# Kernel optimization log

Hardware: AMD Instinct MI355X
Metric: run time of the kernel (lower is better)

The kernel has to match this reference:

```python
import jax, jax.numpy as jnp
import numpy as np

MAX_SEQ_LEN = 128
H = 512
B = 256
S = 128
VOCAB = MAX_SEQ_LEN + 2
SOS = MAX_SEQ_LEN  # start token index in embedding table


def _lstm_cell(x, h, c, w_ih, w_hh, b):
    # PyTorch gate order: i, f, g, o
    z = x @ w_ih.T + h @ w_hh.T + b
    i, f, g, o = jnp.split(z, 4, axis=-1)
    c = jax.nn.sigmoid(f) * c + jax.nn.sigmoid(i) * jnp.tanh(g)
    h = jax.nn.sigmoid(o) * jnp.tanh(c)
    return h, c


def _run_layer(xs, w_ih, w_hh, b):
    nb = xs.shape[1]
    h0 = jnp.zeros((nb, H), xs.dtype)

    def step(carry, x):
        h, c = carry
        h, c = _lstm_cell(x, h, c, w_ih, w_hh, b)
        return (h, c), h

    (hT, cT), ys = jax.lax.scan(step, (h0, h0), xs)
    return ys, hT, cT


def _forward(l2_features, enc, dec, emb, fc1_w, fc1_b, fc2_w, fc2_b, fc3_w, mlp):
    xs = jnp.transpose(l2_features, (1, 0, 2))  # [S,B,F]
    hs, cs = [], []
    for (w_ih, w_hh, b) in enc:  # 3-layer encoder LSTM
        xs, hT, cT = _run_layer(xs, w_ih, w_hh, b)
        hs.append(hT)
        cs.append(cT)
    enc_outs = xs  # [S,B,H]
    h_stack = jnp.stack(hs)  # [3,B,H]
    c_stack = jnp.stack(cs)
    ot = enc_outs @ fc2_w.T + fc2_b  # [S,B,256], loop-invariant
    w1, b1, w2, b2, w3, b3 = mlp
    (dw_ih0, dw_hh0, db0), (dw_ih1, dw_hh1, db1), (dw_ih2, dw_hh2, db2) = dec
    nb = l2_features.shape[0]
    tok0 = jnp.full((nb,), SOS, dtype=jnp.int32)
    ctx0 = jnp.zeros((nb, H), l2_features.dtype)

    def dec_step(carry, _):
        h, c, ctx, tok = carry
        # dropout is identity in eval mode
        x = jnp.concatenate([emb[tok], ctx], axis=1)  # [B, 2H]
        h0, c0 = _lstm_cell(x, h[0], c[0], dw_ih0, dw_hh0, db0)
        h1, c1 = _lstm_cell(h0, h[1], c[1], dw_ih1, dw_hh1, db1)
        h2, c2 = _lstm_cell(h1, h[2], c[2], dw_ih2, dw_hh2, db2)
        ht = h2 @ fc1_w.T + fc1_b  # [B,256]
        scores = jnp.tanh(ot + ht[None]) @ fc3_w[0]  # [S,B]
        w = jax.nn.softmax(scores, axis=0)  # softmax over encoder time (dim 0)
        new_ctx = jnp.einsum('sb,sbd->bd', w, enc_outs)  # [B,H]
        hdd = jax.nn.relu(jnp.concatenate([h2, new_ctx], axis=1) @ w1.T + b1)
        hdd = jax.nn.relu(hdd @ w2.T + b2)
        out = hdd @ w3.T + b3  # [B, MAX_SEQ_LEN]
        new_tok = jnp.argmax(out, axis=-1).astype(jnp.int32)
        new_carry = (jnp.stack([h0, h1, h2]), jnp.stack([c0, c1, c2]), new_ctx, new_tok)
        return new_carry, out

    _, outs = jax.lax.scan(dec_step, (h_stack, c_stack, ctx0, tok0), None, length=MAX_SEQ_LEN)
    return outs  # [MAX_SEQ_LEN, B, MAX_SEQ_LEN]


def setup_inputs() -> dict:
    key = jax.random.key(0)
    ks = iter(jax.random.split(key, 40))

    def p(shape):
        return jax.random.normal(next(ks), shape, dtype=jnp.float32) * 0.05

    d = {"l2_features": jax.random.normal(next(ks), (B, S, MAX_SEQ_LEN), dtype=jnp.float32)}
    d["enc_w_ih0"] = p((4 * H, MAX_SEQ_LEN)); d["enc_w_hh0"] = p((4 * H, H)); d["enc_b0"] = p((4 * H,))
    d["enc_w_ih1"] = p((4 * H, H)); d["enc_w_hh1"] = p((4 * H, H)); d["enc_b1"] = p((4 * H,))
    d["enc_w_ih2"] = p((4 * H, H)); d["enc_w_hh2"] = p((4 * H, H)); d["enc_b2"] = p((4 * H,))
    d["dec_w_ih0"] = p((4 * H, 2 * H)); d["dec_w_hh0"] = p((4 * H, H)); d["dec_b0"] = p((4 * H,))
    d["dec_w_ih1"] = p((4 * H, H)); d["dec_w_hh1"] = p((4 * H, H)); d["dec_b1"] = p((4 * H,))
    d["dec_w_ih2"] = p((4 * H, H)); d["dec_w_hh2"] = p((4 * H, H)); d["dec_b2"] = p((4 * H,))
    d["emb"] = p((VOCAB, H))
    d["fc1_w"] = p((256, H)); d["fc1_b"] = p((256,))
    d["fc2_w"] = p((256, H)); d["fc2_b"] = p((256,))
    d["fc3_w"] = p((1, 256))
    d["mlp_w1"] = p((512, 1024)); d["mlp_b1"] = p((512,))
    d["mlp_w2"] = p((256, 512)); d["mlp_b2"] = p((256,))
    d["mlp_w3"] = p((MAX_SEQ_LEN, 256)); d["mlp_b3"] = p((MAX_SEQ_LEN,))
    return d


def reference(l2_features, enc_w_ih0, enc_w_hh0, enc_b0, enc_w_ih1, enc_w_hh1, enc_b1,
              enc_w_ih2, enc_w_hh2, enc_b2, dec_w_ih0, dec_w_hh0, dec_b0,
              dec_w_ih1, dec_w_hh1, dec_b1, dec_w_ih2, dec_w_hh2, dec_b2,
              emb, fc1_w, fc1_b, fc2_w, fc2_b, fc3_w,
              mlp_w1, mlp_b1, mlp_w2, mlp_b2, mlp_w3, mlp_b3):
    enc = ((enc_w_ih0, enc_w_hh0, enc_b0), (enc_w_ih1, enc_w_hh1, enc_b1), (enc_w_ih2, enc_w_hh2, enc_b2))
    dec = ((dec_w_ih0, dec_w_hh0, dec_b0), (dec_w_ih1, dec_w_hh1, dec_b1), (dec_w_ih2, dec_w_hh2, dec_b2))
    mlp = (mlp_w1, mlp_b1, mlp_w2, mlp_b2, mlp_w3, mlp_b3)
    return _forward(l2_features, enc, dec, emb, fc1_w, fc1_b, fc2_w, fc2_b, fc3_w, mlp)
```

## Files before the change

### kernel.cpp

```cpp
#include <hip/hip_runtime.h>

#define BB 256
#define SS 128
#define FDIM 128
#define HH 512
#define H4 2048
#define TDEC 128
#define SOS_TOK 128

typedef short short8 __attribute__((ext_vector_type(8)));
typedef float f32x4 __attribute__((ext_vector_type(4)));

__device__ __forceinline__ float sigf(float x){ return 1.0f/(1.0f+__expf(-x)); }
__device__ __forceinline__ float tanh_f(float x){ return 1.0f - 2.0f/(__expf(2.0f*x)+1.0f); }

__device__ __forceinline__ void split3(float x, unsigned& h, unsigned& m, unsigned& l){
    union { float f; unsigned u; } a; a.f = x;
    h = (a.u + 0x7fffu + ((a.u>>16)&1u)) >> 16;
    union { unsigned u; float f; } hf; hf.u = h << 16;
    float r1 = x - hf.f;
    union { float f; unsigned u; } b; b.f = r1;
    m = (b.u + 0x7fffu + ((b.u>>16)&1u)) >> 16;
    union { unsigned u; float f; } mf; mf.u = m << 16;
    float r2 = r1 - mf.f;
    union { float f; unsigned u; } c; c.f = r2;
    l = (c.u + 0x7fffu + ((c.u>>16)&1u)) >> 16;
}

__device__ __forceinline__ void splitw8(float4 v, uint2& H, uint2& M, uint2& L){
    unsigned h0,m0,l0,h1,m1,l1,h2,m2,l2,h3,m3,l3;
    split3(v.x,h0,m0,l0); split3(v.y,h1,m1,l1); split3(v.z,h2,m2,l2); split3(v.w,h3,m3,l3);
    H.x = h0 | (h1<<16); H.y = h2 | (h3<<16);
    M.x = m0 | (m1<<16); M.y = m2 | (m3<<16);
    L.x = l0 | (l1<<16); L.y = l2 | (l3<<16);
}

__global__ void split_w(const float* __restrict__ srcA, int KA,
                        const float* __restrict__ srcB, int KB, int ilv,
                        unsigned short* __restrict__ ph, unsigned short* __restrict__ pm,
                        unsigned short* __restrict__ pl, int N){
    int k = blockIdx.x*128 + threadIdx.x;
    int n = blockIdx.y;
    int K = KA + KB;
    if (k >= K) return;
    int row = ilv ? ((n&3)*512 + (n>>2)) : n;
    float w = (k < KA) ? srcA[(size_t)row*KA + k] : srcB[(size_t)row*KB + (k-KA)];
    unsigned h,m,l; split3(w,h,m,l);
    size_t off = (size_t)(k>>5)*((size_t)N*32) + (size_t)n*32
               + ((((k>>3)&3) ^ (n&3))<<3) + (k&7);
    ph[off]=(unsigned short)h; pm[off]=(unsigned short)m; pl[off]=(unsigned short)l;
}

__global__ void repack_b(float* __restrict__ dst, const float* __restrict__ src){
    int id = blockIdx.x*256 + threadIdx.x;
    if (id >= 2048) return;
    int g = id & 3, q = id >> 2;
    dst[id] = src[g*512 + q];
}

__global__ void init_tok(int* __restrict__ tok){ tok[threadIdx.x] = SOS_TOK; }

#define MM6(AH,AM,AL,BH,BM,BL,C) \
  C = __builtin_amdgcn_mfma_f32_16x16x32_bf16(AH,BH,C,0,0,0); \
  C = __builtin_amdgcn_mfma_f32_16x16x32_bf16(AH,BM,C,0,0,0); \
  C = __builtin_amdgcn_mfma_f32_16x16x32_bf16(AM,BH,C,0,0,0); \
  C = __builtin_amdgcn_mfma_f32_16x16x32_bf16(AH,BL,C,0,0,0); \
  C = __builtin_amdgcn_mfma_f32_16x16x32_bf16(AL,BH,C,0,0,0); \
  C = __builtin_amdgcn_mfma_f32_16x16x32_bf16(AM,BM,C,0,0,0);

template<int MODE>
__global__ __launch_bounds__(256) void mg(
    const float* __restrict__ A0, long a0B, long a0T,
    const float* __restrict__ A1, const float* __restrict__ A2,
    const int* __restrict__ tok, int ksh,
    const unsigned short* __restrict__ Wh, const unsigned short* __restrict__ Wm,
    const unsigned short* __restrict__ Wl, int Nld,
    int Kc, int Mrows,
    const float* __restrict__ bias, int relu,
    float* __restrict__ out, long oB, long oT,
    const float* __restrict__ xz, float* __restrict__ c_io, float* __restrict__ seqo)
{
    __shared__ __align__(16) unsigned short sA[2][3][2048];
    __shared__ __align__(16) unsigned short sW[2][3][2048];
    const int tid = threadIdx.x;
    const int row0 = blockIdx.y * 64, col0 = blockIdx.x * 64;
    const int kz = blockIdx.z * Kc;
    const int nk = Kc >> 5;

    f32x4 acc[2][2];
    acc[0][0] = (f32x4){0.f,0.f,0.f,0.f}; acc[0][1] = (f32x4){0.f,0.f,0.f,0.f};
    acc[1][0] = (f32x4){0.f,0.f,0.f,0.f}; acc[1][1] = (f32x4){0.f,0.f,0.f,0.f};

    const int sr = tid >> 2, q4 = tid & 3;
    const int gr = row0 + sr;
    long ro0;
    if (tok){ int rr = tok[gr & 255]; ro0 = (long)rr * a0B; }
    else ro0 = (long)(gr & 255)*a0B + (long)(gr >> 8)*a0T;
    const long ro1 = (long)gr * 512;
    const size_t wbase = (size_t)col0*32 + (size_t)tid*8;
    const int swz = sr & 3;
    const int b0 = sr*32 + (q4 & 1)*4;
    const int p0s = ((q4>>1) ^ swz) << 3;
    const int p1s = ((2 + (q4>>1)) ^ swz) << 3;

    float4 va0, va1; uint4 vw0, vw1, vw2;

    auto issue = [&](int kt){
        int kg = kz + kt*32;
        int seg = kg >> ksh;
        const float* sp = (seg==0)? A0 : ((seg==1)? A1 : A2);
        long ro = (seg==0)? ro0 : ro1;
        int ko = kg & ((1<<ksh)-1);
        const float* p = sp + ro + ko + q4*4;
        va0 = *(const float4*)p;
        va1 = *(const float4*)(p + 16);
        size_t wi = (size_t)(kg>>5)*((size_t)Nld*32) + wbase;
        vw0 = *(const uint4*)(Wh + wi);
        vw1 = *(const uint4*)(Wm + wi);
        vw2 = *(const uint4*)(Wl + wi);
    };
    auto commit = [&](int buf){
        uint2 H,M,L;
        splitw8(va0,H,M,L);
        *(uint2*)&sA[buf][0][b0 + p0s] = H;
        *(uint2*)&sA[buf][1][b0 + p0s] = M;
        *(uint2*)&sA[buf][2][b0 + p0s] = L;
        splitw8(va1,H,M,L);
        *(uint2*)&sA[buf][0][b0 + p1s] = H;
        *(uint2*)&sA[buf][1][b0 + p1s] = M;
        *(uint2*)&sA[buf][2][b0 + p1s] = L;
        *(uint4*)&sW[buf][0][tid*8] = vw0;
        *(uint4*)&sW[buf][1][tid*8] = vw1;
        *(uint4*)&sW[buf][2][tid*8] = vw2;
    };

    const int wid = tid >> 6, lane = tid & 63;
    const int wy = wid >> 1, wx = wid & 1;
    const int l15 = lane & 15, l4 = lane >> 4;
    const int offA = (wy*32 + l15)*32 + ((l4 ^ (l15&3))<<3);
    const int offB = (wx*32 + l15)*32 + ((l4 ^ (l15&3))<<3);

    auto compute = [&](int buf){
        short8 a0h = *(const short8*)&sA[buf][0][offA];
        short8 a0m = *(const short8*)&sA[buf][1][offA];
        short8 a0l = *(const short8*)&sA[buf][2][offA];
        short8 a1h = *(const short8*)&sA[buf][0][offA+512];
        short8 a1m = *(const short8*)&sA[buf][1][offA+512];
        short8 a1l = *(const short8*)&sA[buf][2][offA+512];
        short8 b0h = *(const short8*)&sW[buf][0][offB];
        short8 b0m = *(const short8*)&sW[buf][1][offB];
        short8 b0l = *(const short8*)&sW[buf][2][offB];
        short8 b1h = *(const short8*)&sW[buf][0][offB+512];
        short8 b1m = *(const short8*)&sW[buf][1][offB+512];
        short8 b1l = *(const short8*)&sW[buf][2][offB+512];
        MM6(a0h,a0m,a0l,b0h,b0m,b0l,acc[0][0])
        MM6(a0h,a0m,a0l,b1h,b1m,b1l,acc[0][1])
        MM6(a1h,a1m,a1l,b0h,b0m,b0l,acc[1][0])
        MM6(a1h,a1m,a1l,b1h,b1m,b1l,acc[1][1])
    };

    issue(0);
    commit(0);
    __syncthreads();
    int buf = 0;
    for (int kt=0; kt<nk; ++kt){
        bool more = (kt+1 < nk);
        if (more) issue(kt+1);
        compute(buf);
        if (more) commit(buf^1);
        __syncthreads();
        buf ^= 1;
    }

    if (MODE == 0){
        #pragma unroll
        for (int fa=0; fa<2; fa++){
            #pragma unroll
            for (int fb=0; fb<2; fb++){
                int gc = col0 + wx*32 + fb*16 + l15;
                float bv = bias ? bias[gc] : 0.0f;
                #pragma unroll
                for (int i=0;i<4;i++){
                    int r = row0 + wy*32 + fa*16 + l4*4 + i;
                    float v = acc[fa][fb][i] + bv;
                    if (relu) v = fmaxf(v, 0.0f);
                    out[(size_t)(r&255)*oB + (size_t)(r>>8)*oT + gc] = v;
                }
            }
        }
    } else if (MODE == 1){
        #pragma unroll
        for (int fa=0; fa<2; fa++){
            #pragma unroll
            for (int fb=0; fb<2; fb++){
                int gc = col0 + wx*32 + fb*16 + l15;
                #pragma unroll
                for (int i=0;i<4;i++){
                    int r = row0 + wy*32 + fa*16 + l4*4 + i;
                    out[((size_t)blockIdx.z*Mrows + r)*(size_t)Nld + gc] = acc[fa][fb][i];
                }
            }
        }
    } else {
        #pragma unroll
        for (int fa=0; fa<2; fa++){
            #pragma unroll
            for (int fb=0; fb<2; fb++){
                int gc = col0 + wx*32 + fb*16 + l15;
                int q = gc >> 2, g = gc & 3;
                #pragma unroll
                for (int i=0;i<4;i++){
                    int r = row0 + wy*32 + fa*16 + l4*4 + i;
                    float z = acc[fa][fb][i] + xz[(size_t)r*2048 + gc];
                    float x1 = __shfl_xor(z, 1);
                    float x2 = __shfl_xor(z, 2);
                    float x3 = __shfl_xor(z, 3);
                    float zi = (g==0)?z :(g==1)?x1:(g==2)?x2:x3;
                    float zf = (g==1)?z :(g==0)?x1:(g==3)?x2:x3;
                    float zg = (g==2)?z :(g==3)?x1:(g==0)?x2:x3;
                    float zo = (g==3)?z :(g==2)?x1:(g==1)?x2:x3;
                    float co = c_io[(size_t)r*512 + q];
                    float cn = sigf(zf)*co + sigf(zi)*tanh_f(zg);
                    float hn = sigf(zo)*tanh_f(cn);
                    if (g == 1) c_io[(size_t)r*512 + q] = cn;
                    else if (g == 0) seqo[(size_t)r*512 + q] = hn;
                }
            }
        }
    }
}

__global__ __launch_bounds__(256) void cell_red(
    const float* __restrict__ zp, int KS, const float* __restrict__ bias,
    float* __restrict__ c_io, float* __restrict__ h)
{
    int id = blockIdx.x*256 + threadIdx.x;
    int b = id >> 9, q = id & 511;
    float4 z = *(const float4*)(zp + (size_t)b*2048 + q*4);
    for (int s=1; s<KS; s++){
        float4 t = *(const float4*)(zp + ((size_t)s*256 + b)*2048 + q*4);
        z.x += t.x; z.y += t.y; z.z += t.z; z.w += t.w;
    }
    float4 bb = *(const float4*)(bias + q*4);
    float zi = z.x + bb.x, zf = z.y + bb.y, zg = z.z + bb.z, zo = z.w + bb.w;
    float co = c_io[id];
    float cn = sigf(zf)*co + sigf(zi)*tanh_f(zg);
    float hn = sigf(zo)*tanh_f(cn);
    c_io[id] = cn;
    h[id] = hn;
}

__global__ __launch_bounds__(256) void red1(
    const float* __restrict__ zp, int KS, int ln, const float* __restrict__ bias,
    int relu, float* __restrict__ out)
{
    int id = blockIdx.x*256 + threadIdx.x;
    int b = id >> ln, n = id & ((1<<ln)-1);
    float v = 0.f;
    for (int s=0; s<KS; s++) v += zp[(((size_t)s*256 + b) << ln) + n];
    v += bias[n];
    if (relu) v = fmaxf(v, 0.f);
    out[id] = v;
}

__global__ __launch_bounds__(256) void attn_kernel(
    const float* __restrict__ ht, const float* __restrict__ ot,
    const float* __restrict__ enc, const float* __restrict__ fc3,
    float* __restrict__ ctx)
{
    __shared__ float hts[256], f3s[256], wsm[SS];
    const int b = blockIdx.x, tid = threadIdx.x;
    hts[tid] = ht[(size_t)b*256 + tid];
    f3s[tid] = fc3[tid];
    __syncthreads();
    const int wave = tid >> 6, lane = tid & 63;
    const float* otb = ot + (size_t)b*SS*256;
    for (int i=0;i<32;i++){
        int s = wave*32 + i;
        float4 o = *(const float4*)&otb[(size_t)s*256 + lane*4];
        int d0 = lane*4;
        float v = f3s[d0+0]*tanh_f(o.x + hts[d0+0])
                + f3s[d0+1]*tanh_f(o.y + hts[d0+1])
                + f3s[d0+2]*tanh_f(o.z + hts[d0+2])
                + f3s[d0+3]*tanh_f(o.w + hts[d0+3]);
        #pragma unroll
        for (int off=32; off; off>>=1) v += __shfl_xor(v, off);
        if (lane == 0) wsm[s] = v;
    }
    __syncthreads();
    if (tid < 64){
        float v0 = wsm[tid], v1 = wsm[tid+64];
        float m = fmaxf(v0, v1);
        #pragma unroll
        for (int off=32; off; off>>=1) m = fmaxf(m, __shfl_xor(m, off));
        float e0 = __expf(v0 - m), e1 = __expf(v1 - m);
        float ss = e0 + e1;
        #pragma unroll
        for (int off=32; off; off>>=1) ss += __shfl_xor(ss, off);
        float inv = 1.0f/ss;
        wsm[tid] = e0*inv; wsm[tid+64] = e1*inv;
    }
    __syncthreads();
    float a0=0.f, a1=0.f;
    const float* eb = enc + (size_t)b*HH;
    #pragma unroll 8
    for (int s=0;s<SS;s++){
        float w = wsm[s];
        const float* e = eb + (size_t)s*BB*HH;
        a0 = fmaf(w, e[tid],      a0);
        a1 = fmaf(w, e[tid+256],  a1);
    }
    ctx[(size_t)b*HH + tid]      = a0;
    ctx[(size_t)b*HH + tid+256]  = a1;
}

__global__ __launch_bounds__(64) void argmax_kernel(const float* __restrict__ logits, int* __restrict__ tok){
    const int b = blockIdx.x, lane = threadIdx.x;
    const float* r = logits + (size_t)b*128;
    float v0 = r[lane], v1 = r[lane+64];
    float bv; int bi;
    if (v1 > v0){ bv = v1; bi = lane+64; } else { bv = v0; bi = lane; }
    #pragma unroll
    for (int off=32; off; off>>=1){
        float ov = __shfl_xor(bv, off);
        int   oi = __shfl_xor(bi, off);
        if (ov > bv || (ov == bv && oi < bi)){ bv = ov; bi = oi; }
    }
    if (lane == 0) tok[b] = bi;
}

extern "C" void kernel_launch(void* const* d_in, const int* in_sizes, int n_in,
                              void* d_out, int out_size, void* d_ws, size_t ws_size,
                              hipStream_t stream)
{
    (void)in_sizes; (void)n_in; (void)out_size;
    const float* l2      = (const float*)d_in[0];
    const float* e_wih[3] = {(const float*)d_in[1],(const float*)d_in[4],(const float*)d_in[7]};
    const float* e_whh[3] = {(const float*)d_in[2],(const float*)d_in[5],(const float*)d_in[8]};
    const float* e_b[3]   = {(const float*)d_in[3],(const float*)d_in[6],(const float*)d_in[9]};
    const float* d_wih[3] = {(const float*)d_in[10],(const float*)d_in[13],(const float*)d_in[16]};
    const float* d_whh[3] = {(const float*)d_in[11],(const float*)d_in[14],(const float*)d_in[17]};
    const float* d_b[3]   = {(const float*)d_in[12],(const float*)d_in[15],(const float*)d_in[18]};
    const float* emb   = (const float*)d_in[19];
    const float* fc1_w = (const float*)d_in[20]; const float* fc1_b = (const float*)d_in[21];
    const float* fc2_w = (const float*)d_in[22]; const float* fc2_b = (const float*)d_in[23];
    const float* fc3_w = (const float*)d_in[24];
    const float* w1 = (const float*)d_in[25]; const float* b1 = (const float*)d_in[26];
    const float* w2 = (const float*)d_in[27]; const float* b2 = (const float*)d_in[28];
    const float* w3 = (const float*)d_in[29]; const float* b3 = (const float*)d_in[30];
    float* out = (float*)d_out;

    float* base = (float*)d_ws;
    size_t off = 0;
    auto alloc = [&](size_t n)->float*{ float* r = base + off; off = (off + n + 63) & ~(size_t)63; return r; };

    struct WSpec { const float* a; int ka; const float* b; int kb; int ilv; int n; };
    WSpec ws[14] = {
        {e_wih[0],128, nullptr,0, 1,2048}, {e_wih[1],512, nullptr,0, 1,2048}, {e_wih[2],512, nullptr,0, 1,2048},
        {e_whh[0],512, nullptr,0, 1,2048}, {e_whh[1],512, nullptr,0, 1,2048}, {e_whh[2],512, nullptr,0, 1,2048},
        {d_wih[0],1024, d_whh[0],512, 1,2048}, {d_wih[1],512, d_whh[1],512, 1,2048}, {d_wih[2],512, d_whh[2],512, 1,2048},
        {fc1_w,512, nullptr,0, 0,256}, {fc2_w,512, nullptr,0, 0,256},
        {w1,1024, nullptr,0, 0,512}, {w2,512, nullptr,0, 0,256}, {w3,256, nullptr,0, 0,128}
    };
    unsigned short* wp[14][3];
    for (int i=0;i<14;i++){
        size_t sz = (size_t)(ws[i].ka + ws[i].kb) * ws[i].n;
        float* blk = alloc((sz*3 + 1)/2);
        wp[i][0] = (unsigned short*)blk;
        wp[i][1] = wp[i][0] + sz;
        wp[i][2] = wp[i][0] + 2*sz;
    }
    float* br_e[3]; for (int l=0;l<3;l++) br_e[l] = alloc(2048);
    float* br_d[3]; for (int l=0;l<3;l++) br_d[l] = alloc(2048);

    float* seq   = alloc((size_t)SS*BB*HH);
    float* ot    = alloc((size_t)BB*SS*256);
    float* zpart = alloc((size_t)2*BB*H4);
    float* zbuf  = alloc((size_t)BB*HH);
    float* cbuf[3]; for (int l=0;l<3;l++) cbuf[l] = alloc((size_t)BB*HH);
    float* hbuf[3]; for (int l=0;l<3;l++) hbuf[l] = alloc((size_t)BB*HH);
    float* ctx  = alloc((size_t)BB*HH);
    float* ht   = alloc((size_t)BB*256);
    float* hdd1 = alloc((size_t)BB*512);
    float* hdd2 = alloc((size_t)BB*256);
    int*   tok  = (int*)alloc(256);

    size_t remain = (ws_size/4 > off) ? (ws_size/4 - off) : 0;
    int CH = 4;
    if      (remain >= (size_t)32*BB*H4) CH = 32;
    else if (remain >= (size_t)16*BB*H4) CH = 16;
    else if (remain >= (size_t) 8*BB*H4) CH = 8;
    float* xz = base + off;

    for (int i=0;i<14;i++){
        int K = ws[i].ka + ws[i].kb;
        hipLaunchKernelGGL(split_w, dim3((K+127)/128, ws[i].n), dim3(128), 0, stream,
                           ws[i].a, ws[i].ka, ws[i].b, ws[i].kb, ws[i].ilv,
                           wp[i][0], wp[i][1], wp[i][2], ws[i].n);
    }
    for (int l=0;l<3;l++){
        hipLaunchKernelGGL(repack_b, dim3(8), dim3(256), 0, stream, br_e[l], e_b[l]);
        hipLaunchKernelGGL(repack_b, dim3(8), dim3(256), 0, stream, br_d[l], d_b[l]);
    }
    hipMemsetAsync(zbuf, 0, (size_t)BB*HH*4, stream);
    for (int l=0;l<3;l++) hipMemsetAsync(cbuf[l], 0, (size_t)BB*HH*4, stream);
    hipMemsetAsync(ctx, 0, (size_t)BB*HH*4, stream);

    for (int l=0;l<3;l++){
        const int Kih = (l==0)? FDIM : HH;
        const int wih = l, whhI = 3+l;
        const int nch = SS / CH;
        for (int tc=0; tc<nch; tc++){
            const float* A0; long sB, sT;
            if (l == 0){ A0 = l2 + (size_t)tc*CH*FDIM; sB = (long)SS*FDIM; sT = FDIM; }
            else       { A0 = seq + (size_t)tc*CH*BB*HH; sB = HH; sT = (long)BB*HH; }
            hipLaunchKernelGGL((mg<0>), dim3(32, CH*4, 1), dim3(256), 0, stream,
                A0, sB, sT, (const float*)nullptr, (const float*)nullptr, (const int*)nullptr, 30,
                wp[wih][0], wp[wih][1], wp[wih][2], 2048, Kih, 256,
                br_e[l], 0, xz, (long)H4, (long)BB*H4,
                (const float*)nullptr, (float*)nullptr, (float*)nullptr);
            for (int ti=0; ti<CH; ti++){
                int t = tc*CH + ti;
                const float* hp = (t==0) ? zbuf : seq + (size_t)(t-1)*BB*HH;
                hipLaunchKernelGGL((mg<2>), dim3(32, 4, 1), dim3(256), 0, stream,
                    hp, (long)HH, 0L, (const float*)nullptr, (const float*)nullptr, (const int*)nullptr, 30,
                    wp[whhI][0], wp[whhI][1], wp[whhI][2], 2048, HH, 256,
                    (const float*)nullptr, 0, (float*)nullptr, 0L, 0L,
                    xz + (size_t)ti*BB*H4, cbuf[l], seq + (size_t)t*BB*HH);
            }
        }
        hipMemcpyAsync(hbuf[l], seq + (size_t)(SS-1)*BB*HH, (size_t)BB*HH*4,
                       hipMemcpyDeviceToDevice, stream);
    }

    hipLaunchKernelGGL((mg<0>), dim3(4, 512, 1), dim3(256), 0, stream,
        seq, (long)HH, (long)BB*HH, (const float*)nullptr, (const float*)nullptr, (const int*)nullptr, 30,
        wp[10][0], wp[10][1], wp[10][2], 256, HH, 256,
        fc2_b, 0, ot, (long)SS*256, 256L,
        (const float*)nullptr, (float*)nullptr, (float*)nullptr);

    hipLaunchKernelGGL(init_tok, dim3(1), dim3(256), 0, stream, tok);
    for (int t=0; t<TDEC; t++){
        hipLaunchKernelGGL((mg<1>), dim3(32, 4, 2), dim3(256), 0, stream,
            emb, (long)HH, 0L, ctx, hbuf[0], tok, 9,
            wp[6][0], wp[6][1], wp[6][2], 2048, 768, 256,
            (const float*)nullptr, 0, zpart, 0L, 0L,
            (const float*)nullptr, (float*)nullptr, (float*)nullptr);
        hipLaunchKernelGGL(cell_red, dim3(512), dim3(256), 0, stream, zpart, 2, br_d[0], cbuf[0], hbuf[0]);
        hipLaunchKernelGGL((mg<1>), dim3(32, 4, 2), dim3(256), 0, stream,
            hbuf[0], (long)HH, 0L, hbuf[1], (const float*)nullptr, (const int*)nullptr, 9,
            wp[7][0], wp[7][1], wp[7][2], 2048, 512, 256,
            (const float*)nullptr, 0, zpart, 0L, 0L,
            (const float*)nullptr, (float*)nullptr, (float*)nullptr);
        hipLaunchKernelGGL(cell_red, dim3(512), dim3(256), 0, stream, zpart, 2, br_d[1], cbuf[1], hbuf[1]);
        hipLaunchKernelGGL((mg<1>), dim3(32, 4, 2), dim3(256), 0, stream,
            hbuf[1], (long)HH, 0L, hbuf[2], (const float*)nullptr, (const int*)nullptr, 9,
            wp[8][0], wp[8][1], wp[8][2], 2048, 512, 256,
            (const float*)nullptr, 0, zpart, 0L, 0L,
            (const float*)nullptr, (float*)nullptr, (float*)nullptr);
        hipLaunchKernelGGL(cell_red, dim3(512), dim3(256), 0, stream, zpart, 2, br_d[2], cbuf[2], hbuf[2]);
        hipLaunchKernelGGL((mg<0>), dim3(4, 4, 1), dim3(256), 0, stream,
            hbuf[2], (long)HH, 0L, (const float*)nullptr, (const float*)nullptr, (const int*)nullptr, 30,
            wp[9][0], wp[9][1], wp[9][2], 256, HH, 256,
            fc1_b, 0, ht, 256L, 0L,
            (const float*)nullptr, (float*)nullptr, (float*)nullptr);
        hipLaunchKernelGGL(attn_kernel, dim3(BB), dim3(256), 0, stream, ht, ot, seq, fc3_w, ctx);
        hipLaunchKernelGGL((mg<1>), dim3(8, 4, 4), dim3(256), 0, stream,
            hbuf[2], (long)HH, 0L, ctx, (const float*)nullptr, (const int*)nullptr, 9,
            wp[11][0], wp[11][1], wp[11][2], 512, 256, 256,
            (const float*)nullptr, 0, zpart, 0L, 0L,
            (const float*)nullptr, (float*)nullptr, (float*)nullptr);
        hipLaunchKernelGGL(red1, dim3(512), dim3(256), 0, stream, zpart, 4, 9, b1, 1, hdd1);
        hipLaunchKernelGGL((mg<1>), dim3(4, 4, 4), dim3(256), 0, stream,
            hdd1, 512L, 0L, (const float*)nullptr, (const float*)nullptr, (const int*)nullptr, 30,
            wp[12][0], wp[12][1], wp[12][2], 256, 128, 256,
            (const float*)nullptr, 0, zpart, 0L, 0L,
            (const float*)nullptr, (float*)nullptr, (float*)nullptr);
        hipLaunchKernelGGL(red1, dim3(256), dim3(256), 0, stream, zpart, 4, 8, b2, 1, hdd2);
        hipLaunchKernelGGL((mg<0>), dim3(2, 4, 1), dim3(256), 0, stream,
            hdd2, 256L, 0L, (const float*)nullptr, (const float*)nullptr, (const int*)nullptr, 30,
            wp[13][0], wp[13][1], wp[13][2], 128, 256, 256,
            b3, 0, out + (size_t)t*BB*128, 128L, 0L,
            (const float*)nullptr, (float*)nullptr, (float*)nullptr);
        hipLaunchKernelGGL(argmax_kernel, dim3(BB), dim3(64), 0, stream, out + (size_t)t*BB*128, tok);
    }
}
```

Measured before the change: 27.71 ms.

## Drop to two-term bf16 split and fuse decoder kernels to cut launches

Result: slower. 32.81 ms (+18.4%).

```diff
diff --git a/kernel.cpp b/kernel.cpp
--- a/kernel.cpp
+++ b/kernel.cpp
@@ -14,41 +14,36 @@
 __device__ __forceinline__ float sigf(float x){ return 1.0f/(1.0f+__expf(-x)); }
 __device__ __forceinline__ float tanh_f(float x){ return 1.0f - 2.0f/(__expf(2.0f*x)+1.0f); }
 
-__device__ __forceinline__ void split3(float x, unsigned& h, unsigned& m, unsigned& l){
+__device__ __forceinline__ void split2(float x, unsigned& h, unsigned& m){
     union { float f; unsigned u; } a; a.f = x;
     h = (a.u + 0x7fffu + ((a.u>>16)&1u)) >> 16;
     union { unsigned u; float f; } hf; hf.u = h << 16;
     float r1 = x - hf.f;
     union { float f; unsigned u; } b; b.f = r1;
     m = (b.u + 0x7fffu + ((b.u>>16)&1u)) >> 16;
-    union { unsigned u; float f; } mf; mf.u = m << 16;
-    float r2 = r1 - mf.f;
-    union { float f; unsigned u; } c; c.f = r2;
-    l = (c.u + 0x7fffu + ((c.u>>16)&1u)) >> 16;
-}
-
-__device__ __forceinline__ void splitw8(float4 v, uint2& H, uint2& M, uint2& L){
-    unsigned h0,m0,l0,h1,m1,l1,h2,m2,l2,h3,m3,l3;
-    split3(v.x,h0,m0,l0); split3(v.y,h1,m1,l1); split3(v.z,h2,m2,l2); split3(v.w,h3,m3,l3);
+}
+
+__device__ __forceinline__ void splitw8(float4 v, uint2& H, uint2& M){
+    unsigned h0,m0,h1,m1,h2,m2,h3,m3;
+    split2(v.x,h0,m0); split2(v.y,h1,m1); split2(v.z,h2,m2); split2(v.w,h3,m3);
     H.x = h0 | (h1<<16); H.y = h2 | (h3<<16);
     M.x = m0 | (m1<<16); M.y = m2 | (m3<<16);
-    L.x = l0 | (l1<<16); L.y = l2 | (l3<<16);
 }
 
 __global__ void split_w(const float* __restrict__ srcA, int KA,
                         const float* __restrict__ srcB, int KB, int ilv,
                         unsigned short* __restrict__ ph, unsigned short* __restrict__ pm,
-                        unsigned short* __restrict__ pl, int N){
+                        int N){
     int k = blockIdx.x*128 + threadIdx.x;
     int n = blockIdx.y;
     int K = KA + KB;
     if (k >= K) return;
     int row = ilv ? ((n&3)*512 + (n>>2)) : n;
     float w = (k < KA) ? srcA[(size_t)row*KA + k] : srcB[(size_t)row*KB + (k-KA)];
-    unsigned h,m,l; split3(w,h,m,l);
+    unsigned h,m; split2(w,h,m);
     size_t off = (size_t)(k>>5)*((size_t)N*32) + (size_t)n*32
                + ((((k>>3)&3) ^ (n&3))<<3) + (k&7);
-    ph[off]=(unsigned short)h; pm[off]=(unsigned short)m; pl[off]=(unsigned short)l;
+    ph[off]=(unsigned short)h; pm[off]=(unsigned short)m;
 }
 
 __global__ void repack_b(float* __restrict__ dst, const float* __restrict__ src){
@@ -60,13 +55,10 @@
 
 __global__ void init_tok(int* __restrict__ tok){ tok[threadIdx.x] = SOS_TOK; }
 
-#define MM6(AH,AM,AL,BH,BM,BL,C) \
+#define MM3(AH,AM,BH,BM,C) \
   C = __builtin_amdgcn_mfma_f32_16x16x32_bf16(AH,BH,C,0,0,0); \
   C = __builtin_amdgcn_mfma_f32_16x16x32_bf16(AH,BM,C,0,0,0); \
-  C = __builtin_amdgcn_mfma_f32_16x16x32_bf16(AM,BH,C,0,0,0); \
-  C = __builtin_amdgcn_mfma_f32_16x16x32_bf16(AH,BL,C,0,0,0); \
-  C = __builtin_amdgcn_mfma_f32_16x16x32_bf16(AL,BH,C,0,0,0); \
-  C = __builtin_amdgcn_mfma_f32_16x16x32_bf16(AM,BM,C,0,0,0);
+  C = __builtin_amdgcn_mfma_f32_16x16x32_bf16(AM,BH,C,0,0,0);
 
 template<int MODE>
 __global__ __launch_bounds__(256) void mg(
@@ -74,17 +66,15 @@
     const float* __restrict__ A1, const float* __restrict__ A2,
     const int* __restrict__ tok, int ksh,
     const unsigned short* __restrict__ Wh, const unsigned short* __restrict__ Wm,
-    const unsigned short* __restrict__ Wl, int Nld,
-    int Kc, int Mrows,
+    int Nld, int Kc,
     const float* __restrict__ bias, int relu,
     float* __restrict__ out, long oB, long oT,
     const float* __restrict__ xz, float* __restrict__ c_io, float* __restrict__ seqo)
 {
-    __shared__ __align__(16) unsigned short sA[2][3][2048];
-    __shared__ __align__(16) unsigned short sW[2][3][2048];
+    __shared__ __align__(16) unsigned short sA[2][2][2048];
+    __shared__ __align__(16) unsigned short sW[2][2][2048];
     const int tid = threadIdx.x;
     const int row0 = blockIdx.y * 64, col0 = blockIdx.x * 64;
-    const int kz = blockIdx.z * Kc;
     const int nk = Kc >> 5;
 
     f32x4 acc[2][2];
@@ -103,10 +93,10 @@
     const int p0s = ((q4>>1) ^ swz) << 3;
     const int p1s = ((2 + (q4>>1)) ^ swz) << 3;
 
-    float4 va0, va1; uint4 vw0, vw1, vw2;
+    float4 va0, va1; uint4 vw0, vw1;
 
     auto issue = [&](int kt){
-        int kg = kz + kt*32;
+        int kg = kt*32;
         int seg = kg >> ksh;
         const float* sp = (seg==0)? A0 : ((seg==1)? A1 : A2);
         long ro = (seg==0)? ro0 : ro1;
@@ -117,21 +107,17 @@
         size_t wi = (size_t)(kg>>5)*((size_t)Nld*32) + wbase;
         vw0 = *(const uint4*)(Wh + wi);
         vw1 = *(const uint4*)(Wm + wi);
-        vw2 = *(const uint4*)(Wl + wi);
     };
     auto commit = [&](int buf){
-        uint2 H,M,L;
-        splitw8(va0,H,M,L);
+        uint2 H,M;
+        splitw8(va0,H,M);
         *(uint2*)&sA[buf][0][b0 + p0s] = H;
         *(uint2*)&sA[buf][1][b0 + p0s] = M;
-        *(uint2*)&sA[buf][2][b0 + p0s] = L;
-        splitw8(va1,H,M,L);
+        splitw8(va1,H,M);
         *(uint2*)&sA[buf][0][b0 + p1s] = H;
         *(uint2*)&sA[buf][1][b0 + p1s] = M;
-        *(uint2*)&sA[buf][2][b0 + p1s] = L;
         *(uint4*)&sW[buf][0][tid*8] = vw0;
         *(uint4*)&sW[buf][1][tid*8] = vw1;
-        *(uint4*)&sW[buf][2][tid*8] = vw2;
     };
 
     const int wid = tid >> 6, lane = tid & 63;
@@ -143,20 +129,16 @@
     auto compute = [&](int buf){
         short8 a0h = *(const short8*)&sA[buf][0][offA];
         short8 a0m = *(const short8*)&sA[buf][1][offA];
-        short8 a0l = *(const short8*)&sA[buf][2][offA];
         short8 a1h = *(const short8*)&sA[buf][0][offA+512];
         short8 a1m = *(const short8*)&sA[buf][1][offA+512];
-        short8 a1l = *(const short8*)&sA[buf][2][offA+512];
         short8 b0h = *(const short8*)&sW[buf][0][offB];
         short8 b0m = *(const short8*)&sW[buf][1][offB];
-        short8 b0l = *(const short8*)&sW[buf][2][offB];
         short8 b1h = *(const short8*)&sW[buf][0][offB+512];
         short8 b1m = *(const short8*)&sW[buf][1][offB+512];
-        short8 b1l = *(const short8*)&sW[buf][2][offB+512];
-        MM6(a0h,a0m,a0l,b0h,b0m,b0l,acc[0][0])
-        MM6(a0h,a0m,a0l,b1h,b1m,b1l,acc[0][1])
-        MM6(a1h,a1m,a1l,b0h,b0m,b0l,acc[1][0])
-        MM6(a1h,a1m,a1l,b1h,b1m,b1l,acc[1][1])
+        MM3(a0h,a0m,b0h,b0m,acc[0][0])
+        MM3(a0h,a0m,b1h,b1m,acc[0][1])
+        MM3(a1h,a1m,b0h,b0m,acc[1][0])
+        MM3(a1h,a1m,b1h,b1m,acc[1][1])
     };
 
     issue(0);
@@ -188,19 +170,6 @@
                 }
             }
         }
-    } else if (MODE == 1){
-        #pragma unroll
-        for (int fa=0; fa<2; fa++){
-            #pragma unroll
-            for (int fb=0; fb<2; fb++){
-                int gc = col0 + wx*32 + fb*16 + l15;
-                #pragma unroll
-                for (int i=0;i<4;i++){
-                    int r = row0 + wy*32 + fa*16 + l4*4 + i;
-                    out[((size_t)blockIdx.z*Mrows + r)*(size_t)Nld + gc] = acc[fa][fb][i];
-                }
-            }
-        }
     } else {
         #pragma unroll
         for (int fa=0; fa<2; fa++){
@@ -208,10 +177,12 @@
             for (int fb=0; fb<2; fb++){
                 int gc = col0 + wx*32 + fb*16 + l15;
                 int q = gc >> 2, g = gc & 3;
+                float ab = xz ? 0.0f : bias[gc];
                 #pragma unroll
                 for (int i=0;i<4;i++){
                     int r = row0 + wy*32 + fa*16 + l4*4 + i;
-                    float z = acc[fa][fb][i] + xz[(size_t)r*2048 + gc];
+                    float addv = xz ? xz[(size_t)r*2048 + gc] : ab;
+                    float z = acc[fa][fb][i] + addv;
                     float x1 = __shfl_xor(z, 1);
                     float x2 = __shfl_xor(z, 2);
                     float x3 = __shfl_xor(z, 3);
@@ -230,48 +201,34 @@
     }
 }
 
-__global__ __launch_bounds__(256) void cell_red(
-    const float* __restrict__ zp, int KS, const float* __restrict__ bias,
-    float* __restrict__ c_io, float* __restrict__ h)
-{
-    int id = blockIdx.x*256 + threadIdx.x;
-    int b = id >> 9, q = id & 511;
-    float4 z = *(const float4*)(zp + (size_t)b*2048 + q*4);
-    for (int s=1; s<KS; s++){
-        float4 t = *(const float4*)(zp + ((size_t)s*256 + b)*2048 + q*4);
-        z.x += t.x; z.y += t.y; z.z += t.z; z.w += t.w;
-    }
-    float4 bb = *(const float4*)(bias + q*4);
-    float zi = z.x + bb.x, zf = z.y + bb.y, zg = z.z + bb.z, zo = z.w + bb.w;
-    float co = c_io[id];
-    float cn = sigf(zf)*co + sigf(zi)*tanh_f(zg);
-    float hn = sigf(zo)*tanh_f(cn);
-    c_io[id] = cn;
-    h[id] = hn;
-}
-
-__global__ __launch_bounds__(256) void red1(
-    const float* __restrict__ zp, int KS, int ln, const float* __restrict__ bias,
-    int relu, float* __restrict__ out)
-{
-    int id = blockIdx.x*256 + threadIdx.x;
-    int b = id >> ln, n = id & ((1<<ln)-1);
-    float v = 0.f;
-    for (int s=0; s<KS; s++) v += zp[(((size_t)s*256 + b) << ln) + n];
-    v += bias[n];
-    if (relu) v = fmaxf(v, 0.f);
-    out[id] = v;
-}
-
-__global__ __launch_bounds__(256) void attn_kernel(
-    const float* __restrict__ ht, const float* __restrict__ ot,
-    const float* __restrict__ enc, const float* __restrict__ fc3,
+__global__ __launch_bounds__(256) void attn_fc1(
+    const float* __restrict__ h2,
+    const float* __restrict__ fc1w,
+    const float* __restrict__ fc1b,
+    const float* __restrict__ ot,
+    const float* __restrict__ enc,
+    const float* __restrict__ fc3,
     float* __restrict__ ctx)
 {
-    __shared__ float hts[256], f3s[256], wsm[SS];
+    __shared__ float h2s[512], hts[256], f3s[256], wsm[SS];
     const int b = blockIdx.x, tid = threadIdx.x;
-    hts[tid] = ht[(size_t)b*256 + tid];
+    h2s[tid]     = h2[(size_t)b*512 + tid];
+    h2s[tid+256] = h2[(size_t)b*512 + tid + 256];
     f3s[tid] = fc3[tid];
+    __syncthreads();
+    {
+        const float4* wr = (const float4*)(fc1w + (size_t)tid*512);
+        float s0=0.f, s1=0.f;
+        #pragma unroll 4
+        for (int k4=0; k4<128; k4+=2){
+            float4 w0 = wr[k4], w1 = wr[k4+1];
+            float4 hh0 = *(const float4*)&h2s[k4*4];
+            float4 hh1 = *(const float4*)&h2s[k4*4+4];
+            s0 = fmaf(w0.x,hh0.x,fmaf(w0.y,hh0.y,fmaf(w0.z,hh0.z,fmaf(w0.w,hh0.w,s0))));
+            s1 = fmaf(w1.x,hh1.x,fmaf(w1.y,hh1.y,fmaf(w1.z,hh1.z,fmaf(w1.w,hh1.w,s1))));
+        }
+        hts[tid] = s0 + s1 + fc1b[tid];
+    }
     __syncthreads();
     const int wave = tid >> 6, lane = tid & 63;
     const float* otb = ot + (size_t)b*SS*256;
@@ -314,19 +271,44 @@
     ctx[(size_t)b*HH + tid+256]  = a1;
 }
 
-__global__ __launch_bounds__(64) void argmax_kernel(const float* __restrict__ logits, int* __restrict__ tok){
-    const int b = blockIdx.x, lane = threadIdx.x;
-    const float* r = logits + (size_t)b*128;
-    float v0 = r[lane], v1 = r[lane+64];
-    float bv; int bi;
-    if (v1 > v0){ bv = v1; bi = lane+64; } else { bv = v0; bi = lane; }
-    #pragma unroll
-    for (int off=32; off; off>>=1){
-        float ov = __shfl_xor(bv, off);
-        int   oi = __shfl_xor(bi, off);
-        if (ov > bv || (ov == bv && oi < bi)){ bv = ov; bi = oi; }
-    }
-    if (lane == 0) tok[b] = bi;
+__global__ __launch_bounds__(128) void mlp3_argmax(
+    const float* __restrict__ hdd2,
+    const float* __restrict__ w3,
+    const float* __restrict__ b3,
+    float* __restrict__ outp,
+    int* __restrict__ tok)
+{
+    __shared__ float hs[256], lg[128];
+    const int b = blockIdx.x, tid = threadIdx.x;
+    hs[tid]     = hdd2[(size_t)b*256 + tid];
+    hs[tid+128] = hdd2[(size_t)b*256 + tid + 128];
+    __syncthreads();
+    const float4* wr = (const float4*)(w3 + (size_t)tid*256);
+    float s0=0.f, s1=0.f;
+    #pragma unroll 4
+    for (int k4=0; k4<64; k4+=2){
+        float4 w0 = wr[k4], w1 = wr[k4+1];
+        float4 h0 = *(const float4*)&hs[k4*4];
+        float4 h1 = *(const float4*)&hs[k4*4+4];
+        s0 = fmaf(w0.x,h0.x,fmaf(w0.y,h0.y,fmaf(w0.z,h0.z,fmaf(w0.w,h0.w,s0))));
+        s1 = fmaf(w1.x,h1.x,fmaf(w1.y,h1.y,fmaf(w1.z,h1.z,fmaf(w1.w,h1.w,s1))));
+    }
+    float v = s0 + s1 + b3[tid];
+    outp[(size_t)b*128 + tid] = v;
+    lg[tid] = v;
+    __syncthreads();
+    if (tid < 64){
+        float v0 = lg[tid], v1 = lg[tid+64];
+        float bv; int bi;
+        if (v1 > v0){ bv = v1; bi = tid+64; } else { bv = v0; bi = tid; }
+        #pragma unroll
+        for (int off=32; off; off>>=1){
+            float ov = __shfl_xor(bv, off);
+            int   oi = __shfl_xor(bi, off);
+            if (ov > bv || (ov == bv && oi < bi)){ bv = ov; bi = oi; }
+        }
+        if (tid == 0) tok[b] = bi;
+    }
 }
 
 extern "C" void kernel_launch(void* const* d_in, const int* in_sizes, int n_in,
@@ -355,32 +337,30 @@
     auto alloc = [&](size_t n)->float*{ float* r = base + off; off = (off + n + 63) & ~(size_t)63; return r; };
 
     struct WSpec { const float* a; int ka; const float* b; int kb; int ilv; int n; };
-    WSpec ws[14] = {
+    WSpec ws[13] = {
         {e_wih[0],128, nullptr,0, 1,2048}, {e_wih[1],512, nullptr,0, 1,2048}, {e_wih[2],512, nullptr,0, 1,2048},
         {e_whh[0],512, nullptr,0, 1,2048}, {e_whh[1],512, nullptr,0, 1,2048}, {e_whh[2],512, nullptr,0, 1,2048},
         {d_wih[0],1024, d_whh[0],512, 1,2048}, {d_wih[1],512, d_whh[1],512, 1,2048}, {d_wih[2],512, d_whh[2],512, 1,2048},
-        {fc1_w,512, nullptr,0, 0,256}, {fc2_w,512, nullptr,0, 0,256},
+        {fc2_w,512, nullptr,0, 0,256},
         {w1,1024, nullptr,0, 0,512}, {w2,512, nullptr,0, 0,256}, {w3,256, nullptr,0, 0,128}
     };
-    unsigned short* wp[14][3];
-    for (int i=0;i<14;i++){
+    unsigned short* wp[13][2];
+    for (int i=0;i<13;i++){
         size_t sz = (size_t)(ws[i].ka + ws[i].kb) * ws[i].n;
-        float* blk = alloc((sz*3 + 1)/2);
+        float* blk = alloc(sz);
         wp[i][0] = (unsigned short*)blk;
         wp[i][1] = wp[i][0] + sz;
-        wp[i][2] = wp[i][0] + 2*sz;
     }
     float* br_e[3]; for (int l=0;l<3;l++) br_e[l] = alloc(2048);
     float* br_d[3]; for (int l=0;l<3;l++) br_d[l] = alloc(2048);
 
     float* seq   = alloc((size_t)SS*BB*HH);
     float* ot    = alloc((size_t)BB*SS*256);
-    float* zpart = alloc((size_t)2*BB*H4);
     float* zbuf  = alloc((size_t)BB*HH);
     float* cbuf[3]; for (int l=0;l<3;l++) cbuf[l] = alloc((size_t)BB*HH);
-    float* hbuf[3]; for (int l=0;l<3;l++) hbuf[l] = alloc((size_t)BB*HH);
+    float* hbuf[3][2];
+    for (int l=0;l<3;l++) for (int p=0;p<2;p++) hbuf[l][p] = alloc((size_t)BB*HH);
     float* ctx  = alloc((size_t)BB*HH);
-    float* ht   = alloc((size_t)BB*256);
     float* hdd1 = alloc((size_t)BB*512);
     float* hdd2 = alloc((size_t)BB*256);
     int*   tok  = (int*)alloc(256);
@@ -392,11 +372,11 @@
     else if (remain >= (size_t) 8*BB*H4) CH = 8;
     float* xz = base + off;
 
-    for (int i=0;i<14;i++){
+    for (int i=0;i<13;i++){
         int K = ws[i].ka + ws[i].kb;
         hipLaunchKernelGGL(split_w, dim3((K+127)/128, ws[i].n), dim3(128), 0, stream,
                            ws[i].a, ws[i].ka, ws[i].b, ws[i].kb, ws[i].ilv,
-                           wp[i][0], wp[i][1], wp[i][2], ws[i].n);
+                           wp[i][0], wp[i][1], ws[i].n);
     }
     for (int l=0;l<3;l++){
         hipLaunchKernelGGL(repack_b, dim3(8), dim3(256), 0, stream, br_e[l], e_b[l]);
@@ -408,80 +388,67 @@
 
     for (int l=0;l<3;l++){
         const int Kih = (l==0)? FDIM : HH;
-        const int wih = l, whhI = 3+l;
         const int nch = SS / CH;
         for (int tc=0; tc<nch; tc++){
             const float* A0; long sB, sT;
             if (l == 0){ A0 = l2 + (size_t)tc*CH*FDIM; sB = (long)SS*FDIM; sT = FDIM; }
             else       { A0 = seq + (size_t)tc*CH*BB*HH; sB = HH; sT = (long)BB*HH; }
-            hipLaunchKernelGGL((mg<0>), dim3(32, CH*4, 1), dim3(256), 0, stream,
+            hipLaunchKernelGGL((mg<0>), dim3(32, CH*4), dim3(256), 0, stream,
                 A0, sB, sT, (const float*)nullptr, (const float*)nullptr, (const int*)nullptr, 30,
-                wp[wih][0], wp[wih][1], wp[wih][2], 2048, Kih, 256,
+                wp[l][0], wp[l][1], 2048, Kih,
                 br_e[l], 0, xz, (long)H4, (long)BB*H4,
                 (const float*)nullptr, (float*)nullptr, (float*)nullptr);
             for (int ti=0; ti<CH; ti++){
                 int t = tc*CH + ti;
                 const float* hp = (t==0) ? zbuf : seq + (size_t)(t-1)*BB*HH;
-                hipLaunchKernelGGL((mg<2>), dim3(32, 4, 1), dim3(256), 0, stream,
+                hipLaunchKernelGGL((mg<2>), dim3(32, 4), dim3(256), 0, stream,
                     hp, (long)HH, 0L, (const float*)nullptr, (const float*)nullptr, (const int*)nullptr, 30,
-                    wp[whhI][0], wp[whhI][1], wp[whhI][2], 2048, HH, 256,
+                    wp[3+l][0], wp[3+l][1], 2048, HH,
                     (const float*)nullptr, 0, (float*)nullptr, 0L, 0L,
                     xz + (size_t)ti*BB*H4, cbuf[l], seq + (size_t)t*BB*HH);
             }
         }
-        hipMemcpyAsync(hbuf[l], seq + (size_t)(SS-1)*BB*HH, (size_t)BB*HH*4,
+        hipMemcpyAsync(hbuf[l][0], seq + (size_t)(SS-1)*BB*HH, (size_t)BB*HH*4,
                        hipMemcpyDeviceToDevice, stream);
     }
 
-    hipLaunchKernelGGL((mg<0>), dim3(4, 512, 1), dim3(256), 0, stream,
+    hipLaunchKernelGGL((mg<0>), dim3(4, 512), dim3(256), 0, stream,
         seq, (long)HH, (long)BB*HH, (const float*)nullptr, (const float*)nullptr, (const int*)nullptr, 30,
-        wp[10][0], wp[10][1], wp[10][2], 256, HH, 256,
+        wp[9][0], wp[9][1], 256, HH,
         fc2_b, 0, ot, (long)SS*256, 256L,
         (const float*)nullptr, (float*)nullptr, (float*)nullptr);
 
     hipLaunchKernelGGL(init_tok, dim3(1), dim3(256), 0, stream, tok);
     for (int t=0; t<TDEC; t++){
-        hipLaunchKernelGGL((mg<1>), dim3(32, 4, 2), dim3(256), 0, stream,
-            emb, (long)HH, 0L, ctx, hbuf[0], tok, 9,
-            wp[6][0], wp[6][1], wp[6][2], 2048, 768, 256,
-            (const float*)nullptr, 0, zpart, 0L, 0L,
+        const int p = t & 1;
+        hipLaunchKernelGGL((mg<2>), dim3(32, 4), dim3(256), 0, stream,
+            emb, (long)HH, 0L, ctx, hbuf[0][p], tok, 9,
+            wp[6][0], wp[6][1], 2048, 3*HH,
+            br_d[0], 0, (float*)nullptr, 0L, 0L,
+            (const float*)nullptr, cbuf[0], hbuf[0][p^1]);
+        hipLaunchKernelGGL((mg<2>), dim3(32, 4), dim3(256), 0, stream,
+            hbuf[0][p^1], (long)HH, 0L, hbuf[1][p], (const float*)nullptr, (const int*)nullptr, 9,
+            wp[7][0], wp[7][1], 2048, 2*HH,
+            br_d[1], 0, (float*)nullptr, 0L, 0L,
+            (const float*)nullptr, cbuf[1], hbuf[1][p^1]);
+        hipLaunchKernelGGL((mg<2>), dim3(32, 4), dim3(256), 0, stream,
+            hbuf[1][p^1], (long)HH, 0L, hbuf[2][p], (const float*)nullptr, (const int*)nullptr, 9,
+            wp[8][0], wp[8][1], 2048, 2*HH,
+            br_d[2], 0, (float*)nullptr, 0L, 0L,
+            (const float*)nullptr, cbuf[2], hbuf[2][p^1]);
+        hipLaunchKernelGGL(attn_fc1, dim3(BB), dim3(256), 0, stream,
+            hbuf[2][p^1], fc1_w, fc1_b, ot, seq, fc3_w, ctx);
+        hipLaunchKernelGGL((mg<0>), dim3(8, 4), dim3(256), 0, stream,
+            hbuf[2][p^1], (long)HH, 0L, ctx, (const float*)nullptr, (const int*)nullptr, 9,
+            wp[10][0], wp[10][1], 512, 2*HH,
+            b1, 1, hdd1, 512L, 0L,
             (const float*)nullptr, (float*)nullptr, (float*)nullptr);
-        hipLaunchKernelGGL(cell_red, dim3(512), dim3(256), 0, stream, zpart, 2, br_d[0], cbuf[0], hbuf[0]);
-        hipLaunchKernelGGL((mg<1>), dim3(32, 4, 2), dim3(256), 0, stream,
-            hbuf[0], (long)HH, 0L, hbuf[1], (const float*)nullptr, (const int*)nullptr, 9,
-            wp[7][0], wp[7][1], wp[7][2], 2048, 512, 256,
-            (const float*)nullptr, 0, zpart, 0L, 0L,
+        hipLaunchKernelGGL((mg<0>), dim3(4, 4), dim3(256), 0, stream,
+            hdd1, 512L, 0L, (const float*)nullptr, (const float*)nullptr, (const int*)nullptr, 30,
+            wp[11][0], wp[11][1], 256, HH,
+            b2, 1, hdd2, 256L, 0L,
             (const float*)nullptr, (float*)nullptr, (float*)nullptr);
-        hipLaunchKernelGGL(cell_red, dim3(512), dim3(256), 0, stream, zpart, 2, br_d[1], cbuf[1], hbuf[1]);
-        hipLaunchKernelGGL((mg<1>), dim3(32, 4, 2), dim3(256), 0, stream,
-            hbuf[1], (long)HH, 0L, hbuf[2], (const float*)nullptr, (const int*)nullptr, 9,
-            wp[8][0], wp[8][1], wp[8][2], 2048, 512, 256,
-            (const float*)nullptr, 0, zpart, 0L, 0L,
-            (const float*)nullptr, (float*)nullptr, (float*)nullptr);
-        hipLaunchKernelGGL(cell_red, dim3(512), dim3(256), 0, stream, zpart, 2, br_d[2], cbuf[2], hbuf[2]);
-        hipLaunchKernelGGL((mg<0>), dim3(4, 4, 1), dim3(256), 0, stream,
-            hbuf[2], (long)HH, 0L, (const float*)nullptr, (const float*)nullptr, (const int*)nullptr, 30,
-            wp[9][0], wp[9][1], wp[9][2], 256, HH, 256,
-            fc1_b, 0, ht, 256L, 0L,
-            (const float*)nullptr, (float*)nullptr, (float*)nullptr);
-        hipLaunchKernelGGL(attn_kernel, dim3(BB), dim3(256), 0, stream, ht, ot, seq, fc3_w, ctx);
-        hipLaunchKernelGGL((mg<1>), dim3(8, 4, 4), dim3(256), 0, stream,
-            hbuf[2], (long)HH, 0L, ctx, (const float*)nullptr, (const int*)nullptr, 9,
-            wp[11][0], wp[11][1], wp[11][2], 512, 256, 256,
-            (const float*)nullptr, 0, zpart, 0L, 0L,
-            (const float*)nullptr, (float*)nullptr, (float*)nullptr);
-        hipLaunchKernelGGL(red1, dim3(512), dim3(256), 0, stream, zpart, 4, 9, b1, 1, hdd1);
-        hipLaunchKernelGGL((mg<1>), dim3(4, 4, 4), dim3(256), 0, stream,
-            hdd1, 512L, 0L, (const float*)nullptr, (const float*)nullptr, (const int*)nullptr, 30,
-            wp[12][0], wp[12][1], wp[12][2], 256, 128, 256,
-            (const float*)nullptr, 0, zpart, 0L, 0L,
-            (const float*)nullptr, (float*)nullptr, (float*)nullptr);
-        hipLaunchKernelGGL(red1, dim3(256), dim3(256), 0, stream, zpart, 4, 8, b2, 1, hdd2);
-        hipLaunchKernelGGL((mg<0>), dim3(2, 4, 1), dim3(256), 0, stream,
-            hdd2, 256L, 0L, (const float*)nullptr, (const float*)nullptr, (const int*)nullptr, 30,
-            wp[13][0], wp[13][1], wp[13][2], 128, 256, 256,
-            b3, 0, out + (size_t)t*BB*128, 128L, 0L,
-            (const float*)nullptr, (float*)nullptr, (float*)nullptr);
-        hipLaunchKernelGGL(argmax_kernel, dim3(BB), dim3(64), 0, stream, out + (size_t)t*BB*128, tok);
-    }
-}
+        hipLaunchKernelGGL(mlp3_argmax, dim3(BB), dim3(128), 0, stream,
+            hdd2, w3, b3, out + (size_t)t*BB*128, tok);
+    }
+}
```
